# Optimization experiments

Hardware: AMD Instinct MI355X
Metric: run time of the kernel (lower is better)

Reference implementation:

```python
import jax, jax.numpy as jnp
import numpy as np

N = 1024
H = 256
W = 256
TILE = 16
FX = 300.0
FY = 300.0
CX = 128.0
CY = 128.0
NEAR = 0.1
FAR = 100.0
FRUSTUM_R = 1.0      # cfg.frustum_culling_radius
TILE_CULL_R = 3.0    # cfg.tile_culling_radius (bcircle path)
T_THRESH = 1e-4      # cfg.T_thresh
N_TH = H // TILE
N_TW = W // TILE


def quat_to_rot(q):
    # q: [N,4] (w,x,y,z), normalized inside
    q = q / jnp.linalg.norm(q, axis=-1, keepdims=True)
    w, x, y, z = q[:, 0], q[:, 1], q[:, 2], q[:, 3]
    r0 = jnp.stack([1 - 2 * (y * y + z * z), 2 * (x * y - w * z), 2 * (x * z + w * y)], -1)
    r1 = jnp.stack([2 * (x * y + w * z), 1 - 2 * (x * x + z * z), 2 * (y * z - w * x)], -1)
    r2 = jnp.stack([2 * (x * z - w * y), 2 * (y * z + w * x), 1 - 2 * (x * x + y * y)], -1)
    return jnp.stack([r0, r1, r2], axis=1)  # [N,3,3]


def setup_inputs() -> dict:
    key = jax.random.key(0)
    ks = jax.random.split(key, 6)
    # place gaussians inside the view frustum: depth 2..6, normalized xy in +-0.4
    nxy = jax.random.uniform(ks[0], (N, 2), minval=-0.4, maxval=0.4, dtype=jnp.float32)
    z = jax.random.uniform(ks[1], (N, 1), minval=2.0, maxval=6.0, dtype=jnp.float32)
    mean = jnp.concatenate([nxy * z, z], axis=1)  # [N,3]
    qvec = jax.random.normal(ks[2], (N, 4), dtype=jnp.float32)
    log_svec = jnp.float32(np.log(0.02)) + 0.3 * jax.random.normal(ks[3], (N, 3), dtype=jnp.float32)
    color = jax.random.uniform(ks[4], (N, 3), dtype=jnp.float32)
    alpha = 2.0 * jax.random.normal(ks[5], (N,), dtype=jnp.float32)
    c2w = jnp.concatenate([jnp.eye(3, dtype=jnp.float32), jnp.zeros((3, 1), jnp.float32)], axis=1)
    return {"mean": mean, "qvec": qvec, "log_svec": log_svec, "color": color, "alpha": alpha, "c2w": c2w}


def reference(mean, qvec, log_svec, color, alpha, c2w):
    svec = jnp.exp(log_svec)                      # [N,3]
    a = jax.nn.sigmoid(alpha)                     # [N]
    Rcw = c2w[:, :3]                              # camera->world rotation (cols x,y,z)
    t = c2w[:, 3]
    # world -> camera: p_cam = Rcw^T (p - t) == (p - t) @ Rcw
    mean_cam = (mean - t) @ Rcw                   # [N,3]
    depth = mean_cam[:, 2]
    zc = jnp.maximum(depth, 1e-6)
    inv_z = 1.0 / zc
    x, y = mean_cam[:, 0], mean_cam[:, 1]
    mx, my = x * inv_z, y * inv_z                 # 2D mean in camera-plane units
    # projection Jacobian J [N,2,3]
    zero = jnp.zeros_like(inv_z)
    J = jnp.stack([jnp.stack([inv_z, zero, -x * inv_z * inv_z], -1),
                   jnp.stack([zero, inv_z, -y * inv_z * inv_z], -1)], axis=1)
    Rq = quat_to_rot(qvec)                        # [N,3,3]
    cov3d = jnp.einsum('nij,nj,nkj->nik', Rq, svec * svec, Rq)
    JW = jnp.einsum('nij,kj->nik', J, Rcw)        # J @ Rcw^T (world->cam rot)
    cov = jnp.einsum('nij,njk,nlk->nil', JW, cov3d, JW)  # [N,2,2]
    cov = (cov + jnp.swapaxes(cov, -1, -2)) / 2.0
    c00, c01, c11 = cov[:, 0, 0], cov[:, 0, 1], cov[:, 1, 1]
    m = (c00 + c11) / 2.0
    det = c00 * c11 - c01 * c01
    radius = jax.lax.stop_gradient(jnp.sqrt(m + jnp.sqrt(jnp.clip(m * m - det, 0.0))))
    # --- frustum culling (no-grad boolean mask, bounding-sphere style) ---
    r3d = FRUSTUM_R * jnp.max(svec, axis=-1)
    half_w = (W / 2.0) / FX
    half_h = (H / 2.0) / FY
    marg = r3d * inv_z
    maskf = ((depth > NEAR) & (depth < FAR) &
             (jnp.abs(mx) < half_w + marg) & (jnp.abs(my) < half_h + marg))
    maskf = jax.lax.stop_gradient(maskf)
    # --- per-tile bcircle culling mask ---
    psx, psy = 1.0 / FX, 1.0 / FY
    tlx, tly = -CX / FX, -CY / FY
    tx0 = tlx + jnp.arange(N_TW, dtype=jnp.float32) * TILE * psx
    tx1 = tx0 + TILE * psx
    ty0 = tly + jnp.arange(N_TH, dtype=jnp.float32) * TILE * psy
    ty1 = ty0 + TILE * psy
    smx, smy = jax.lax.stop_gradient(mx), jax.lax.stop_gradient(my)
    dxt = jnp.maximum(jnp.maximum(tx0[None, :] - smx[:, None], smx[:, None] - tx1[None, :]), 0.0)  # [N,ntw]
    dyt = jnp.maximum(jnp.maximum(ty0[None, :] - smy[:, None], smy[:, None] - ty1[None, :]), 0.0)  # [N,nth]
    r2 = (radius * TILE_CULL_R) ** 2
    tmask = (dxt[:, None, :] ** 2 + dyt[:, :, None] ** 2) <= r2[:, None, None]  # [N,nth,ntw]
    tmask = jnp.repeat(jnp.repeat(tmask, TILE, axis=1), TILE, axis=2)           # [N,H,W]
    # --- per-pixel gaussian weights ---
    detc = jnp.maximum(det, 1e-12)
    ia, ib, ic = c11 / detc, -c01 / detc, c00 / detc   # inverse 2x2 cov
    px = tlx + (jnp.arange(W, dtype=jnp.float32) + 0.5) * psx
    py = tly + (jnp.arange(H, dtype=jnp.float32) + 0.5) * psy
    dx = px[None, :] - mx[:, None]                 # [N,W]
    dy = py[None, :] - my[:, None]                 # [N,H]
    quad = (ia[:, None, None] * (dx * dx)[:, None, :]
            + 2.0 * ib[:, None, None] * dy[:, :, None] * dx[:, None, :]
            + ic[:, None, None] * (dy * dy)[:, :, None])      # [N,H,W]
    G = jnp.exp(-0.5 * quad)
    w = a[:, None, None] * G * maskf[:, None, None].astype(G.dtype) * tmask.astype(G.dtype)
    # --- global depth sort (per-tile order == global order restricted to tile) ---
    skey = jnp.where(maskf, jax.lax.stop_gradient(depth), jnp.float32(1e10))
    order = jnp.argsort(skey)
    w = w[order]
    color_s = color[order]
    # --- front-to-back alpha compositing with early-termination mask ---
    Tcum = jnp.cumprod(1.0 - w, axis=0)
    Tprev = jnp.concatenate([jnp.ones((1, H, W), w.dtype), Tcum[:-1]], axis=0)
    weight = jnp.where(Tprev > T_THRESH, Tprev * w, 0.0)
    out = jnp.einsum('nhw,nc->hwc', weight, color_s)   # [H,W,3]
    return out
```

## Files before the change

kernel.cpp:

```cpp
#include <hip/hip_runtime.h>
#include <hip/hip_bf16.h>
#include <math.h>

#define GN      1024
#define GH      256
#define GW      256
#define GTILE   16
#define N_TW    (GW / GTILE)
#define N_TH    (GH / GTILE)
#define FXc     300.0f
#define FYc     300.0f
#define CXc     128.0f
#define CYc     128.0f
#define NEARc   0.1f
#define FARc    100.0f
#define T_TH    0.0001f
#define PSX     (1.0f / FXc)
#define PSY     (1.0f / FYc)
#define TLX     (-CXc / FXc)
#define TLY     (-CYc / FYc)
#define HALF_W  (GW * 0.5f / FXc)
#define HALF_H  (GH * 0.5f / FYc)

#define NT      512

__global__ __launch_bounds__(NT) void splat_all(
    const float* __restrict__ mean, const float* __restrict__ qvec,
    const float* __restrict__ lsv,  const float* __restrict__ color,
    const float* __restrict__ alpha, const float* __restrict__ c2w,
    float* __restrict__ out)
{
    __shared__ float  S1x[GN], S1y[GN], S1d[GN];
    __shared__ int    S1i[GN];
    __shared__ float  skey[GN];
    __shared__ float4 uP0[GN];
    __shared__ float4 uP1[GN];
    __shared__ float  uP2[GN];
    __shared__ int    sord[GN];
    __shared__ int    scnt[16];

    const int tid  = threadIdx.x;
    const int lane = tid & 63;
    const int wv   = tid >> 6;

    float R[3][3], t[3];
#pragma unroll
    for (int r = 0; r < 3; ++r) {
        R[r][0] = c2w[r * 4 + 0];
        R[r][1] = c2w[r * 4 + 1];
        R[r][2] = c2w[r * 4 + 2];
        t[r]    = c2w[r * 4 + 3];
    }

    const float tx0 = TLX + (float)blockIdx.x * (GTILE * PSX);
    const float tx1 = tx0 + GTILE * PSX;
    const float ty0 = TLY + (float)blockIdx.y * (GTILE * PSY);
    const float ty1 = ty0 + GTILE * PSY;

    float s_xc[2], s_yc[2], s_dep[2];
    bool  s_keep[2];

#pragma unroll
    for (int c = 0; c < 2; ++c) {
        const int i = c * NT + tid;
        const float m0 = mean[i * 3 + 0] - t[0];
        const float m1 = mean[i * 3 + 1] - t[1];
        const float m2 = mean[i * 3 + 2] - t[2];
        const float l0 = lsv[i * 3 + 0];
        const float l1 = lsv[i * 3 + 1];
        const float l2 = lsv[i * 3 + 2];

        const float xc    = m0 * R[0][0] + m1 * R[1][0] + m2 * R[2][0];
        const float yc    = m0 * R[0][1] + m1 * R[1][1] + m2 * R[2][1];
        const float depth = m0 * R[0][2] + m1 * R[1][2] + m2 * R[2][2];

        const float zc = fmaxf(depth, 1e-6f);
        const float iz = 1.0f / zc;
        const float mx = xc * iz, my = yc * iz;

        const float r3d  = __expf(fmaxf(l0, fmaxf(l1, l2)));
        const float marg = r3d * iz;
        const bool maskf = (depth > NEARc) && (depth < FARc) &&
                           (fabsf(mx) < HALF_W + marg) && (fabsf(my) < HALF_H + marg);

        const float rb2 = 9.45f * r3d * r3d * iz * iz * (2.0f + mx * mx + my * my);

        const float dxt = fmaxf(fmaxf(tx0 - mx, mx - tx1), 0.0f);
        const float dyt = fmaxf(fmaxf(ty0 - my, my - ty1), 0.0f);

        s_xc[c] = xc; s_yc[c] = yc; s_dep[c] = depth;
        s_keep[c] = maskf && (dxt * dxt + dyt * dyt <= rb2);
    }

    unsigned long long bm[2];
#pragma unroll
    for (int c = 0; c < 2; ++c) {
        bm[c] = __ballot(s_keep[c]);
        if (lane == 0) scnt[c * 8 + wv] = __popcll(bm[c]);
    }
    __syncthreads();

    int cnt[16];
#pragma unroll
    for (int k = 0; k < 16; ++k) cnt[k] = scnt[k];
    int chunkbase[3];
    chunkbase[0] = 0;
#pragma unroll
    for (int c = 0; c < 2; ++c) {
        int s = 0;
#pragma unroll
        for (int w2 = 0; w2 < 8; ++w2) s += cnt[c * 8 + w2];
        chunkbase[c + 1] = chunkbase[c] + s;
    }
    const int n1 = chunkbase[2];

#pragma unroll
    for (int c = 0; c < 2; ++c) {
        if (s_keep[c]) {
            int off = chunkbase[c];
            for (int w2 = 0; w2 < wv; ++w2) off += cnt[c * 8 + w2];
            off += __popcll(bm[c] & ((1ull << lane) - 1ull));
            S1x[off] = s_xc[c];
            S1y[off] = s_yc[c];
            S1d[off] = s_dep[c];
            S1i[off] = c * NT + tid;
        }
    }
    __syncthreads();

    int s2base = 0;
    for (int base = 0; base < n1; base += NT) {
        const int tt = base + tid;
        bool keep2 = false;
        float depth = 0.f, mx = 0.f, my = 0.f, ia = 0.f, ib = 0.f, ic = 0.f;
        float aa = 0.f, cr0 = 0.f, cg0 = 0.f, cb0 = 0.f;
        if (tt < n1) {
            const float xc = S1x[tt];
            const float yc = S1y[tt];
            depth = S1d[tt];
            const int idx = S1i[tt];

            const float zc = fmaxf(depth, 1e-6f);
            const float iz = 1.0f / zc;
            mx = xc * iz; my = yc * iz;

            const float4 q4 = ((const float4*)qvec)[idx];
            const float l0 = lsv[idx * 3 + 0];
            const float l1 = lsv[idx * 3 + 1];
            const float l2 = lsv[idx * 3 + 2];
            const float al = alpha[idx];
            cr0 = color[idx * 3 + 0];
            cg0 = color[idx * 3 + 1];
            cb0 = color[idx * 3 + 2];

            float qw = q4.x, qx = q4.y, qy = q4.z, qz = q4.w;
            const float qinv = 1.0f / sqrtf(qw * qw + qx * qx + qy * qy + qz * qz);
            qw *= qinv; qx *= qinv; qy *= qinv; qz *= qinv;
            float Rq[3][3];
            Rq[0][0] = 1.0f - 2.0f * (qy * qy + qz * qz);
            Rq[0][1] = 2.0f * (qx * qy - qw * qz);
            Rq[0][2] = 2.0f * (qx * qz + qw * qy);
            Rq[1][0] = 2.0f * (qx * qy + qw * qz);
            Rq[1][1] = 1.0f - 2.0f * (qx * qx + qz * qz);
            Rq[1][2] = 2.0f * (qy * qz - qw * qx);
            Rq[2][0] = 2.0f * (qx * qz - qw * qy);
            Rq[2][1] = 2.0f * (qy * qz + qw * qx);
            Rq[2][2] = 1.0f - 2.0f * (qx * qx + qy * qy);

            const float s0 = __expf(l0);
            const float s1 = __expf(l1);
            const float s2 = __expf(l2);
            const float v0 = s0 * s0, v1 = s1 * s1, v2 = s2 * s2;

            float V[3][3];
#pragma unroll
            for (int a = 0; a < 3; ++a)
#pragma unroll
                for (int b = 0; b < 3; ++b)
                    V[a][b] = Rq[a][0] * v0 * Rq[b][0] + Rq[a][1] * v1 * Rq[b][1] +
                              Rq[a][2] * v2 * Rq[b][2];

            float J[2][3];
            J[0][0] = iz;   J[0][1] = 0.0f; J[0][2] = -xc * iz * iz;
            J[1][0] = 0.0f; J[1][1] = iz;   J[1][2] = -yc * iz * iz;

            float JW[2][3];
#pragma unroll
            for (int r = 0; r < 2; ++r)
#pragma unroll
                for (int k = 0; k < 3; ++k)
                    JW[r][k] = J[r][0] * R[k][0] + J[r][1] * R[k][1] + J[r][2] * R[k][2];

            float M[2][3];
#pragma unroll
            for (int r = 0; r < 2; ++r)
#pragma unroll
                for (int cc = 0; cc < 3; ++cc)
                    M[r][cc] = JW[r][0] * V[0][cc] + JW[r][1] * V[1][cc] + JW[r][2] * V[2][cc];
            const float cov00 = M[0][0] * JW[0][0] + M[0][1] * JW[0][1] + M[0][2] * JW[0][2];
            const float cov01 = M[0][0] * JW[1][0] + M[0][1] * JW[1][1] + M[0][2] * JW[1][2];
            const float cov10 = M[1][0] * JW[0][0] + M[1][1] * JW[0][1] + M[1][2] * JW[0][2];
            const float cov11 = M[1][0] * JW[1][0] + M[1][1] * JW[1][1] + M[1][2] * JW[1][2];

            const float c00 = cov00;
            const float c01 = 0.5f * (cov01 + cov10);
            const float c11 = cov11;

            const float mm  = 0.5f * (c00 + c11);
            const float det = c00 * c11 - c01 * c01;
            const float radius = sqrtf(mm + sqrtf(fmaxf(mm * mm - det, 0.0f)));

            const float r3d  = fmaxf(s0, fmaxf(s1, s2));
            const float marg = r3d * iz;
            const bool maskf = (depth > NEARc) && (depth < FARc) &&
                               (fabsf(mx) < HALF_W + marg) && (fabsf(my) < HALF_H + marg);

            const float detc = fmaxf(det, 1e-12f);
            const float idet = 1.0f / detc;
            ia =  c11 * idet;
            ib = -c01 * idet;
            ic =  c00 * idet;

            const float sg = 1.0f / (1.0f + __expf(-al));
            aa = maskf ? sg : 0.0f;
            const float rr = radius * 3.0f;
            const float r2 = rr * rr;

            const float dxt = fmaxf(fmaxf(tx0 - mx, mx - tx1), 0.0f);
            const float dyt = fmaxf(fmaxf(ty0 - my, my - ty1), 0.0f);
            keep2 = (aa > 0.0f) && (dxt * dxt + dyt * dyt <= r2);
        }

        const unsigned long long b2 = __ballot(keep2);
        if (lane == 0) scnt[wv] = __popcll(b2);
        __syncthreads();
        int off = s2base;
        for (int w2 = 0; w2 < wv; ++w2) off += scnt[w2];
        int ctot = 0;
#pragma unroll
        for (int w2 = 0; w2 < 8; ++w2) ctot += scnt[w2];
        if (keep2) {
            const int p = off + __popcll(b2 & ((1ull << lane) - 1ull));
            skey[p] = depth;
            uP0[p]  = make_float4(mx, my, ia, ib);
            uP1[p]  = make_float4(ic, aa, cr0, cg0);
            uP2[p]  = cb0;
        }
        s2base += ctot;
        __syncthreads();
    }
    const int n2 = s2base;

    for (int tt = tid; tt < n2; tt += NT) {
        const float k = skey[tt];
        int rank = 0;
        for (int j = 0; j < n2; ++j) {
            const float kj = skey[j];
            rank += (kj < k) || (kj == k && j < tt);
        }
        sord[rank] = tt;
    }
    __syncthreads();

    if (tid < 256) {
        const int tx = tid & 15;
        const int ty = tid >> 4;
        const int wp = blockIdx.x * GTILE + tx;
        const int hp = blockIdx.y * GTILE + ty;
        const float px = TLX + ((float)wp + 0.5f) * PSX;
        const float py = TLY + ((float)hp + 0.5f) * PSY;

        float T = 1.0f, cr = 0.0f, cg = 0.0f, cb = 0.0f;

        for (int s = 0; s < n2; ++s) {
            const int p = sord[s];
            const float4 p0 = uP0[p];
            const float4 p1 = uP1[p];
            const float cbv = uP2[p];
            const float dx = px - p0.x, dy = py - p0.y;
            const float quad = p0.z * dx * dx + 2.0f * p0.w * dx * dy + p1.x * dy * dy;
            const float G = __expf(-0.5f * quad);
            const float w = p1.y * G;
            const float wt = (T > T_TH) ? T * w : 0.0f;
            cr += wt * p1.z;
            cg += wt * p1.w;
            cb += wt * cbv;
            T *= (1.0f - w);
        }

        const int o = (hp * GW + wp) * 3;
        out[o + 0] = cr;
        out[o + 1] = cg;
        out[o + 2] = cb;
    }
}

extern "C" void kernel_launch(void* const* d_in, const int* in_sizes, int n_in,
                              void* d_out, int out_size, void* d_ws, size_t ws_size,
                              hipStream_t stream) {
    const float* mean  = (const float*)d_in[0];
    const float* qvec  = (const float*)d_in[1];
    const float* lsv   = (const float*)d_in[2];
    const float* color = (const float*)d_in[3];
    const float* alpha = (const float*)d_in[4];
    const float* c2w   = (const float*)d_in[5];
    float* out = (float*)d_out;

    hipLaunchKernelGGL(splat_all, dim3(N_TW, N_TH), dim3(NT), 0, stream,
                       mean, qvec, lsv, color, alpha, c2w, out);
}
```

Measured before the change: 11.62 us.

## Use 1024-thread blocks so each thread handles exactly one gaussian

Raises the block size from 512 to 1024 threads so every gaussian maps to one thread. This removes the two-chunk culling loop, the loop over stage-two batches, and the strided rank-sort loop, along with their extra barriers and prefix-sum bookkeeping. In exchange, each block holds more registers and waves, which may limit occupancy. Compositing still uses only 256 threads, so three quarters of the block sit idle in that phase.

```diff
diff --git a/kernel.cpp b/kernel.cpp
--- a/kernel.cpp
+++ b/kernel.cpp
@@ -22,7 +22,7 @@
 #define HALF_W  (GW * 0.5f / FXc)
 #define HALF_H  (GH * 0.5f / FYc)
 
-#define NT      512
+#define NT      1024
 
 __global__ __launch_bounds__(NT) void splat_all(
     const float* __restrict__ mean, const float* __restrict__ qvec,
@@ -57,208 +57,186 @@
     const float ty0 = TLY + (float)blockIdx.y * (GTILE * PSY);
     const float ty1 = ty0 + GTILE * PSY;
 
-    float s_xc[2], s_yc[2], s_dep[2];
-    bool  s_keep[2];
-
-#pragma unroll
-    for (int c = 0; c < 2; ++c) {
-        const int i = c * NT + tid;
-        const float m0 = mean[i * 3 + 0] - t[0];
-        const float m1 = mean[i * 3 + 1] - t[1];
-        const float m2 = mean[i * 3 + 2] - t[2];
-        const float l0 = lsv[i * 3 + 0];
-        const float l1 = lsv[i * 3 + 1];
-        const float l2 = lsv[i * 3 + 2];
-
-        const float xc    = m0 * R[0][0] + m1 * R[1][0] + m2 * R[2][0];
-        const float yc    = m0 * R[0][1] + m1 * R[1][1] + m2 * R[2][1];
-        const float depth = m0 * R[0][2] + m1 * R[1][2] + m2 * R[2][2];
-
-        const float zc = fmaxf(depth, 1e-6f);
-        const float iz = 1.0f / zc;
-        const float mx = xc * iz, my = yc * iz;
-
-        const float r3d  = __expf(fmaxf(l0, fmaxf(l1, l2)));
-        const float marg = r3d * iz;
-        const bool maskf = (depth > NEARc) && (depth < FARc) &&
-                           (fabsf(mx) < HALF_W + marg) && (fabsf(my) < HALF_H + marg);
-
-        const float rb2 = 9.45f * r3d * r3d * iz * iz * (2.0f + mx * mx + my * my);
-
-        const float dxt = fmaxf(fmaxf(tx0 - mx, mx - tx1), 0.0f);
-        const float dyt = fmaxf(fmaxf(ty0 - my, my - ty1), 0.0f);
-
-        s_xc[c] = xc; s_yc[c] = yc; s_dep[c] = depth;
-        s_keep[c] = maskf && (dxt * dxt + dyt * dyt <= rb2);
-    }
-
-    unsigned long long bm[2];
-#pragma unroll
-    for (int c = 0; c < 2; ++c) {
-        bm[c] = __ballot(s_keep[c]);
-        if (lane == 0) scnt[c * 8 + wv] = __popcll(bm[c]);
-    }
+    const int i = tid;
+    const float m0 = mean[i * 3 + 0] - t[0];
+    const float m1 = mean[i * 3 + 1] - t[1];
+    const float m2 = mean[i * 3 + 2] - t[2];
+    const float l0 = lsv[i * 3 + 0];
+    const float l1 = lsv[i * 3 + 1];
+    const float l2 = lsv[i * 3 + 2];
+
+    const float xc    = m0 * R[0][0] + m1 * R[1][0] + m2 * R[2][0];
+    const float yc    = m0 * R[0][1] + m1 * R[1][1] + m2 * R[2][1];
+    const float depth = m0 * R[0][2] + m1 * R[1][2] + m2 * R[2][2];
+
+    const float zc = fmaxf(depth, 1e-6f);
+    const float iz = 1.0f / zc;
+    const float mx = xc * iz, my = yc * iz;
+
+    const float r3d  = __expf(fmaxf(l0, fmaxf(l1, l2)));
+    const float marg = r3d * iz;
+    const bool maskf = (depth > NEARc) && (depth < FARc) &&
+                       (fabsf(mx) < HALF_W + marg) && (fabsf(my) < HALF_H + marg);
+
+    const float rb2 = 9.45f * r3d * r3d * iz * iz * (2.0f + mx * mx + my * my);
+
+    const float dxt1 = fmaxf(fmaxf(tx0 - mx, mx - tx1), 0.0f);
+    const float dyt1 = fmaxf(fmaxf(ty0 - my, my - ty1), 0.0f);
+    const bool keep1 = maskf && (dxt1 * dxt1 + dyt1 * dyt1 <= rb2);
+
+    const unsigned long long bm = __ballot(keep1);
+    if (lane == 0) scnt[wv] = __popcll(bm);
     __syncthreads();
 
     int cnt[16];
 #pragma unroll
     for (int k = 0; k < 16; ++k) cnt[k] = scnt[k];
-    int chunkbase[3];
-    chunkbase[0] = 0;
-#pragma unroll
-    for (int c = 0; c < 2; ++c) {
-        int s = 0;
-#pragma unroll
-        for (int w2 = 0; w2 < 8; ++w2) s += cnt[c * 8 + w2];
-        chunkbase[c + 1] = chunkbase[c] + s;
-    }
-    const int n1 = chunkbase[2];
-
-#pragma unroll
-    for (int c = 0; c < 2; ++c) {
-        if (s_keep[c]) {
-            int off = chunkbase[c];
-            for (int w2 = 0; w2 < wv; ++w2) off += cnt[c * 8 + w2];
-            off += __popcll(bm[c] & ((1ull << lane) - 1ull));
-            S1x[off] = s_xc[c];
-            S1y[off] = s_yc[c];
-            S1d[off] = s_dep[c];
-            S1i[off] = c * NT + tid;
-        }
-    }
-    __syncthreads();
-
-    int s2base = 0;
-    for (int base = 0; base < n1; base += NT) {
-        const int tt = base + tid;
-        bool keep2 = false;
-        float depth = 0.f, mx = 0.f, my = 0.f, ia = 0.f, ib = 0.f, ic = 0.f;
-        float aa = 0.f, cr0 = 0.f, cg0 = 0.f, cb0 = 0.f;
-        if (tt < n1) {
-            const float xc = S1x[tt];
-            const float yc = S1y[tt];
-            depth = S1d[tt];
-            const int idx = S1i[tt];
-
-            const float zc = fmaxf(depth, 1e-6f);
-            const float iz = 1.0f / zc;
-            mx = xc * iz; my = yc * iz;
-
-            const float4 q4 = ((const float4*)qvec)[idx];
-            const float l0 = lsv[idx * 3 + 0];
-            const float l1 = lsv[idx * 3 + 1];
-            const float l2 = lsv[idx * 3 + 2];
-            const float al = alpha[idx];
-            cr0 = color[idx * 3 + 0];
-            cg0 = color[idx * 3 + 1];
-            cb0 = color[idx * 3 + 2];
-
-            float qw = q4.x, qx = q4.y, qy = q4.z, qz = q4.w;
-            const float qinv = 1.0f / sqrtf(qw * qw + qx * qx + qy * qy + qz * qz);
-            qw *= qinv; qx *= qinv; qy *= qinv; qz *= qinv;
-            float Rq[3][3];
-            Rq[0][0] = 1.0f - 2.0f * (qy * qy + qz * qz);
-            Rq[0][1] = 2.0f * (qx * qy - qw * qz);
-            Rq[0][2] = 2.0f * (qx * qz + qw * qy);
-            Rq[1][0] = 2.0f * (qx * qy + qw * qz);
-            Rq[1][1] = 1.0f - 2.0f * (qx * qx + qz * qz);
-            Rq[1][2] = 2.0f * (qy * qz - qw * qx);
-            Rq[2][0] = 2.0f * (qx * qz - qw * qy);
-            Rq[2][1] = 2.0f * (qy * qz + qw * qx);
-            Rq[2][2] = 1.0f - 2.0f * (qx * qx + qy * qy);
-
-            const float s0 = __expf(l0);
-            const float s1 = __expf(l1);
-            const float s2 = __expf(l2);
-            const float v0 = s0 * s0, v1 = s1 * s1, v2 = s2 * s2;
-
-            float V[3][3];
-#pragma unroll
-            for (int a = 0; a < 3; ++a)
-#pragma unroll
-                for (int b = 0; b < 3; ++b)
-                    V[a][b] = Rq[a][0] * v0 * Rq[b][0] + Rq[a][1] * v1 * Rq[b][1] +
-                              Rq[a][2] * v2 * Rq[b][2];
-
-            float J[2][3];
-            J[0][0] = iz;   J[0][1] = 0.0f; J[0][2] = -xc * iz * iz;
-            J[1][0] = 0.0f; J[1][1] = iz;   J[1][2] = -yc * iz * iz;
-
-            float JW[2][3];
-#pragma unroll
-            for (int r = 0; r < 2; ++r)
-#pragma unroll
-                for (int k = 0; k < 3; ++k)
-                    JW[r][k] = J[r][0] * R[k][0] + J[r][1] * R[k][1] + J[r][2] * R[k][2];
-
-            float M[2][3];
-#pragma unroll
-            for (int r = 0; r < 2; ++r)
-#pragma unroll
-                for (int cc = 0; cc < 3; ++cc)
-                    M[r][cc] = JW[r][0] * V[0][cc] + JW[r][1] * V[1][cc] + JW[r][2] * V[2][cc];
-            const float cov00 = M[0][0] * JW[0][0] + M[0][1] * JW[0][1] + M[0][2] * JW[0][2];
-            const float cov01 = M[0][0] * JW[1][0] + M[0][1] * JW[1][1] + M[0][2] * JW[1][2];
-            const float cov10 = M[1][0] * JW[0][0] + M[1][1] * JW[0][1] + M[1][2] * JW[0][2];
-            const float cov11 = M[1][0] * JW[1][0] + M[1][1] * JW[1][1] + M[1][2] * JW[1][2];
-
-            const float c00 = cov00;
-            const float c01 = 0.5f * (cov01 + cov10);
-            const float c11 = cov11;
-
-            const float mm  = 0.5f * (c00 + c11);
-            const float det = c00 * c11 - c01 * c01;
-            const float radius = sqrtf(mm + sqrtf(fmaxf(mm * mm - det, 0.0f)));
-
-            const float r3d  = fmaxf(s0, fmaxf(s1, s2));
-            const float marg = r3d * iz;
-            const bool maskf = (depth > NEARc) && (depth < FARc) &&
-                               (fabsf(mx) < HALF_W + marg) && (fabsf(my) < HALF_H + marg);
-
-            const float detc = fmaxf(det, 1e-12f);
-            const float idet = 1.0f / detc;
-            ia =  c11 * idet;
-            ib = -c01 * idet;
-            ic =  c00 * idet;
-
-            const float sg = 1.0f / (1.0f + __expf(-al));
-            aa = maskf ? sg : 0.0f;
-            const float rr = radius * 3.0f;
-            const float r2 = rr * rr;
-
-            const float dxt = fmaxf(fmaxf(tx0 - mx, mx - tx1), 0.0f);
-            const float dyt = fmaxf(fmaxf(ty0 - my, my - ty1), 0.0f);
-            keep2 = (aa > 0.0f) && (dxt * dxt + dyt * dyt <= r2);
-        }
-
-        const unsigned long long b2 = __ballot(keep2);
-        if (lane == 0) scnt[wv] = __popcll(b2);
-        __syncthreads();
-        int off = s2base;
-        for (int w2 = 0; w2 < wv; ++w2) off += scnt[w2];
-        int ctot = 0;
-#pragma unroll
-        for (int w2 = 0; w2 < 8; ++w2) ctot += scnt[w2];
-        if (keep2) {
-            const int p = off + __popcll(b2 & ((1ull << lane) - 1ull));
-            skey[p] = depth;
-            uP0[p]  = make_float4(mx, my, ia, ib);
-            uP1[p]  = make_float4(ic, aa, cr0, cg0);
-            uP2[p]  = cb0;
-        }
-        s2base += ctot;
-        __syncthreads();
-    }
-    const int n2 = s2base;
-
-    for (int tt = tid; tt < n2; tt += NT) {
-        const float k = skey[tt];
+    int off1 = 0, n1 = 0;
+#pragma unroll
+    for (int w2 = 0; w2 < 16; ++w2) {
+        off1 += (w2 < wv) ? cnt[w2] : 0;
+        n1   += cnt[w2];
+    }
+
+    if (keep1) {
+        const int p = off1 + __popcll(bm & ((1ull << lane) - 1ull));
+        S1x[p] = xc;
+        S1y[p] = yc;
+        S1d[p] = depth;
+        S1i[p] = i;
+    }
+    __syncthreads();
+
+    bool keep2 = false;
+    float w_dep = 0.f, w_mx = 0.f, w_my = 0.f, w_ia = 0.f, w_ib = 0.f, w_ic = 0.f;
+    float w_aa = 0.f, w_cr = 0.f, w_cg = 0.f, w_cb = 0.f;
+    if (tid < n1) {
+        const float xc2 = S1x[tid];
+        const float yc2 = S1y[tid];
+        const float dep = S1d[tid];
+        const int   idx = S1i[tid];
+
+        const float zc2 = fmaxf(dep, 1e-6f);
+        const float iz2 = 1.0f / zc2;
+        const float mx2 = xc2 * iz2, my2 = yc2 * iz2;
+
+        const float4 q4 = ((const float4*)qvec)[idx];
+        const float k0 = lsv[idx * 3 + 0];
+        const float k1 = lsv[idx * 3 + 1];
+        const float k2 = lsv[idx * 3 + 2];
+        const float al = alpha[idx];
+        w_cr = color[idx * 3 + 0];
+        w_cg = color[idx * 3 + 1];
+        w_cb = color[idx * 3 + 2];
+
+        float qw = q4.x, qx = q4.y, qy = q4.z, qz = q4.w;
+        const float qinv = 1.0f / sqrtf(qw * qw + qx * qx + qy * qy + qz * qz);
+        qw *= qinv; qx *= qinv; qy *= qinv; qz *= qinv;
+        float Rq[3][3];
+        Rq[0][0] = 1.0f - 2.0f * (qy * qy + qz * qz);
+        Rq[0][1] = 2.0f * (qx * qy - qw * qz);
+        Rq[0][2] = 2.0f * (qx * qz + qw * qy);
+        Rq[1][0] = 2.0f * (qx * qy + qw * qz);
+        Rq[1][1] = 1.0f - 2.0f * (qx * qx + qz * qz);
+        Rq[1][2] = 2.0f * (qy * qz - qw * qx);
+        Rq[2][0] = 2.0f * (qx * qz - qw * qy);
+        Rq[2][1] = 2.0f * (qy * qz + qw * qx);
+        Rq[2][2] = 1.0f - 2.0f * (qx * qx + qy * qy);
+
+        const float s0 = __expf(k0);
+        const float s1 = __expf(k1);
+        const float s2 = __expf(k2);
+        const float v0 = s0 * s0, v1 = s1 * s1, v2 = s2 * s2;
+
+        float V[3][3];
+#pragma unroll
+        for (int a = 0; a < 3; ++a)
+#pragma unroll
+            for (int b = 0; b < 3; ++b)
+                V[a][b] = Rq[a][0] * v0 * Rq[b][0] + Rq[a][1] * v1 * Rq[b][1] +
+                          Rq[a][2] * v2 * Rq[b][2];
+
+        float J[2][3];
+        J[0][0] = iz2;  J[0][1] = 0.0f; J[0][2] = -xc2 * iz2 * iz2;
+        J[1][0] = 0.0f; J[1][1] = iz2;  J[1][2] = -yc2 * iz2 * iz2;
+
+        float JW[2][3];
+#pragma unroll
+        for (int r = 0; r < 2; ++r)
+#pragma unroll
+            for (int k = 0; k < 3; ++k)
+                JW[r][k] = J[r][0] * R[k][0] + J[r][1] * R[k][1] + J[r][2] * R[k][2];
+
+        float M[2][3];
+#pragma unroll
+        for (int r = 0; r < 2; ++r)
+#pragma unroll
+            for (int cc = 0; cc < 3; ++cc)
+                M[r][cc] = JW[r][0] * V[0][cc] + JW[r][1] * V[1][cc] + JW[r][2] * V[2][cc];
+        const float cov00 = M[0][0] * JW[0][0] + M[0][1] * JW[0][1] + M[0][2] * JW[0][2];
+        const float cov01 = M[0][0] * JW[1][0] + M[0][1] * JW[1][1] + M[0][2] * JW[1][2];
+        const float cov10 = M[1][0] * JW[0][0] + M[1][1] * JW[0][1] + M[1][2] * JW[0][2];
+        const float cov11 = M[1][0] * JW[1][0] + M[1][1] * JW[1][1] + M[1][2] * JW[1][2];
+
+        const float c00 = cov00;
+        const float c01 = 0.5f * (cov01 + cov10);
+        const float c11 = cov11;
+
+        const float mm  = 0.5f * (c00 + c11);
+        const float det = c00 * c11 - c01 * c01;
+        const float radius = sqrtf(mm + sqrtf(fmaxf(mm * mm - det, 0.0f)));
+
+        const float r3d2  = fmaxf(s0, fmaxf(s1, s2));
+        const float marg2 = r3d2 * iz2;
+        const bool mask2 = (dep > NEARc) && (dep < FARc) &&
+                           (fabsf(mx2) < HALF_W + marg2) && (fabsf(my2) < HALF_H + marg2);
+
+        const float detc = fmaxf(det, 1e-12f);
+        const float idet = 1.0f / detc;
+        w_ia =  c11 * idet;
+        w_ib = -c01 * idet;
+        w_ic =  c00 * idet;
+
+        const float sg = 1.0f / (1.0f + __expf(-al));
+        w_aa = mask2 ? sg : 0.0f;
+        const float rr = radius * 3.0f;
+        const float r2 = rr * rr;
+
+        const float dxt = fmaxf(fmaxf(tx0 - mx2, mx2 - tx1), 0.0f);
+        const float dyt = fmaxf(fmaxf(ty0 - my2, my2 - ty1), 0.0f);
+        keep2 = (w_aa > 0.0f) && (dxt * dxt + dyt * dyt <= r2);
+        w_dep = dep; w_mx = mx2; w_my = my2;
+    }
+
+    const unsigned long long b2 = __ballot(keep2);
+    if (lane == 0) scnt[wv] = __popcll(b2);
+    __syncthreads();
+
+    int off2 = 0, n2 = 0;
+#pragma unroll
+    for (int w2 = 0; w2 < 16; ++w2) {
+        const int cc2 = scnt[w2];
+        off2 += (w2 < wv) ? cc2 : 0;
+        n2   += cc2;
+    }
+
+    if (keep2) {
+        const int p = off2 + __popcll(b2 & ((1ull << lane) - 1ull));
+        skey[p] = w_dep;
+        uP0[p]  = make_float4(w_mx, w_my, w_ia, w_ib);
+        uP1[p]  = make_float4(w_ic, w_aa, w_cr, w_cg);
+        uP2[p]  = w_cb;
+    }
+    __syncthreads();
+
+    if (tid < n2) {
+        const float k = skey[tid];
         int rank = 0;
         for (int j = 0; j < n2; ++j) {
             const float kj = skey[j];
-            rank += (kj < k) || (kj == k && j < tt);
+            rank += (kj < k) || (kj == k && j < tid);
         }
-        sord[rank] = tt;
+        sord[rank] = tid;
     }
     __syncthreads();
 
```

After: 11.12 us. -4.3%, faster.
